# Kernel tuning notes

Hardware: AMD Instinct MI355X
Metric: run time of the kernel (lower is better)

Reference implementation:

```python
import jax, jax.numpy as jnp
import numpy as np

NS, NM, NR, H = 5000, 100000, 2000, 128
E_SM, E_RM, E_SIM, L = 2_000_000, 1_000_000, 2_000_000, 500_000
NUM_LAYERS = 4  # flattened: layer-0 sage convs 0..3, layer-1 sage convs 0..3 -> stacked [2,4,...]


def _seg_sum(x, idx, n):
    return jax.ops.segment_sum(x, idx, num_segments=n)


def sage_conv(x_src, x_dst, Wl, bl, Wr, src, dst, n_dst):
    # PyG SAGEConv: mean-aggregate neighbor features, lin_l (with bias), + lin_r(root, no bias)
    agg = _seg_sum(x_src[src], dst, n_dst)                      # [n_dst, H]
    cnt = _seg_sum(jnp.ones_like(src, dtype=x_src.dtype), dst, n_dst)
    mean = agg / jnp.maximum(cnt, 1.0)[:, None]
    return mean @ Wl + bl + x_dst @ Wr


def gcn_conv(x, W, b, src, dst, n):
    # PyG GCNConv: add self loops, symmetric normalization deg^-1/2 (deg over dst incl. self loops)
    loop = jnp.arange(n, dtype=src.dtype)
    src2 = jnp.concatenate([src, loop])
    dst2 = jnp.concatenate([dst, loop])
    deg = _seg_sum(jnp.ones_like(dst2, dtype=x.dtype), dst2, n)
    dinv = jnp.where(deg > 0, jax.lax.rsqrt(deg), 0.0)
    norm = dinv[src2] * dinv[dst2]                               # [E+n]
    xw = x @ W                                                   # [n, H]
    out = _seg_sum(xw[src2] * norm[:, None], dst2, n)
    return out + b


def setup_inputs() -> dict:
    key = jax.random.key(0)
    ks = jax.random.split(key, 20)
    s = 0.05
    inp = {
        "emb_srna": jax.random.normal(ks[0], (NS, H), jnp.float32) * s,
        "emb_mrna": jax.random.normal(ks[1], (NM, H), jnp.float32) * s,
        "emb_rbp": jax.random.normal(ks[2], (NR, H), jnp.float32) * s,
        # stacked SAGE params: [layer=2, rel=4, ...]; rel order:
        # 0: srna->mrna, 1: mrna->srna (rev), 2: rbp->mrna, 3: mrna->rbp (rev)
        "sage_Wl": jax.random.normal(ks[3], (2, 4, H, H), jnp.float32) * s,
        "sage_bl": jnp.zeros((2, 4, H), jnp.float32),
        "sage_Wr": jax.random.normal(ks[4], (2, 4, H, H), jnp.float32) * s,
        # stacked GCN params: [layer=2, rel=2 (sim, rev_sim), ...]
        "gcn_W": jax.random.normal(ks[5], (2, 2, H, H), jnp.float32) * s,
        "gcn_b": jnp.zeros((2, 2, H), jnp.float32),
        "src_sm": jax.random.randint(ks[6], (E_SM,), 0, NS),
        "dst_sm": jax.random.randint(ks[7], (E_SM,), 0, NM),
        "src_rm": jax.random.randint(ks[8], (E_RM,), 0, NR),
        "dst_rm": jax.random.randint(ks[9], (E_RM,), 0, NM),
        "src_sim": jax.random.randint(ks[10], (E_SIM,), 0, NM),
        "dst_sim": jax.random.randint(ks[11], (E_SIM,), 0, NM),
        "lbl_srna": jax.random.randint(ks[12], (L,), 0, NS),
        "lbl_mrna": jax.random.randint(ks[13], (L,), 0, NM),
        "lbl_rbp": jax.random.randint(ks[14], (L,), 0, NR),
    }
    return inp


def reference(emb_srna, emb_mrna, emb_rbp, sage_Wl, sage_bl, sage_Wr, gcn_W, gcn_b,
              src_sm, dst_sm, src_rm, dst_rm, src_sim, dst_sim,
              lbl_srna, lbl_mrna, lbl_rbp):
    x_s, x_m, x_r = emb_srna, emb_mrna, emb_rbp
    for l in range(2):
        m_new = (
            sage_conv(x_s, x_m, sage_Wl[l, 0], sage_bl[l, 0], sage_Wr[l, 0], src_sm, dst_sm, NM)
            + sage_conv(x_r, x_m, sage_Wl[l, 2], sage_bl[l, 2], sage_Wr[l, 2], src_rm, dst_rm, NM)
            + gcn_conv(x_m, gcn_W[l, 0], gcn_b[l, 0], src_sim, dst_sim, NM)
            + gcn_conv(x_m, gcn_W[l, 1], gcn_b[l, 1], dst_sim, src_sim, NM)
        )
        s_new = sage_conv(x_m, x_s, sage_Wl[l, 1], sage_bl[l, 1], sage_Wr[l, 1], dst_sm, src_sm, NS)
        r_new = sage_conv(x_m, x_r, sage_Wl[l, 3], sage_bl[l, 3], sage_Wr[l, 3], dst_rm, src_rm, NR)
        x_s, x_m, x_r = jax.nn.relu(s_new), jax.nn.relu(m_new), jax.nn.relu(r_new)
    feat_m = x_m[lbl_mrna]
    pred_srna_mrna = jnp.sum(x_s[lbl_srna] * feat_m, axis=-1)
    pred_rbp_mrna = jnp.sum(x_r[lbl_rbp] * feat_m, axis=-1)
    return (pred_srna_mrna, pred_rbp_mrna)
```

## Files before the change

### kernel.cpp

```cpp
#include <hip/hip_runtime.h>
#include <hip/hip_bf16.h>

#define NSN 5000
#define NMN 100000
#define NRN 2000
#define HDIM 128
#define ESM 2000000
#define ERM 1000000
#define ESIM 2000000
#define LBL 500000

#define CNT_TOTAL (4 * NMN + NSN + NRN)
#define POOL_TOTAL (2 * ESM + 2 * ERM + 2 * ESIM)
#define NBTOT 1222
#define WCAP 14336
#define MAXNODES 512
#define MBLK 25000
#define SR_TOTAL (NSN + NRN)

#define CAP0 12288
#define CAP1 8192
#define CAP2 7168
#define CAP3 9216
#define CAP4 12288
#define CAP5 12288
#define PB0 0
#define PB1 (PB0 + 196 * CAP0)
#define PB2 (PB1 + 313 * CAP1)
#define PB3 (PB2 + 196 * CAP2)
#define PB4 (PB3 + 125 * CAP3)
#define PB5 (PB4 + 196 * CAP4)

typedef short bf16x8 __attribute__((ext_vector_type(8)));
typedef float f32x4 __attribute__((ext_vector_type(4)));
typedef float f32x2 __attribute__((ext_vector_type(2)));

__device__ __forceinline__ unsigned short f2bf(float f) {
  unsigned u = __float_as_uint(f);
  unsigned r = (u + 0x7fffu + ((u >> 16) & 1u)) >> 16;
  return (unsigned short)r;
}
__device__ __forceinline__ float bf_lo(unsigned v) { return __uint_as_float(v << 16); }
__device__ __forceinline__ float bf_hi(unsigned v) { return __uint_as_float(v & 0xffff0000u); }
__device__ __forceinline__ unsigned pack2(float x, float y) {
  return (unsigned)f2bf(x) | ((unsigned)f2bf(y) << 16);
}
__device__ __forceinline__ f32x2 up2(unsigned v) {
  f32x2 r;
  r.x = bf_lo(v);
  r.y = bf_hi(v);
  return r;
}
__device__ __forceinline__ void unpack8(uint4 v, float* f) {
  f[0] = bf_lo(v.x); f[1] = bf_hi(v.x);
  f[2] = bf_lo(v.y); f[3] = bf_hi(v.y);
  f[4] = bf_lo(v.z); f[5] = bf_hi(v.z);
  f[6] = bf_lo(v.w); f[7] = bf_hi(v.w);
}


__global__ void zero_int(int* __restrict__ p, int n) {
  int i = blockIdx.x * blockDim.x + threadIdx.x;
  if (i < n) p[i] = 0;
}

struct BInfo { int g; int ns; int ne; };
__device__ __forceinline__ BInfo binfo(int id) {
  BInfo bi;
  if (id < 196)       { int k = id;        bi.g = 0;                   bi.ns = k << 9; bi.ne = min(bi.ns + 512, NMN); }
  else if (id < 509)  { int k = id - 196;  bi.g = NMN;                 bi.ns = k << 4; bi.ne = min(bi.ns + 16,  NSN); }
  else if (id < 705)  { int k = id - 509;  bi.g = NMN + NSN;           bi.ns = k << 9; bi.ne = min(bi.ns + 512, NMN); }
  else if (id < 830)  { int k = id - 705;  bi.g = 2 * NMN + NSN;       bi.ns = k << 4; bi.ne = min(bi.ns + 16,  NRN); }
  else if (id < 1026) { int k = id - 830;  bi.g = 2 * NMN + NSN + NRN; bi.ns = k << 9; bi.ne = min(bi.ns + 512, NMN); }
  else                { int k = id - 1026; bi.g = 3 * NMN + NSN + NRN; bi.ns = k << 9; bi.ne = min(bi.ns + 512, NMN); }
  return bi;
}

__device__ __forceinline__ int pstart(int id) {
  if (id < 196)       return PB0 + id * CAP0;
  else if (id < 509)  return PB1 + (id - 196) * CAP1;
  else if (id < 705)  return PB2 + (id - 509) * CAP2;
  else if (id < 830)  return PB3 + (id - 705) * CAP3;
  else if (id < 1026) return PB4 + (id - 830) * CAP4;
  else                return PB5 + (id - 1026) * CAP5;
}

__global__ void init_pcur(int* __restrict__ bcur) {
  int id = blockIdx.x * blockDim.x + threadIdx.x;
  if (id < NBTOT) bcur[id] = pstart(id);
}

template <int SHF, int NBF, int SHR, int NBR>
__global__ __launch_bounds__(256) void multisplit(
    const int* __restrict__ a, const int* __restrict__ b, int n,
    int* __restrict__ bcur, int bb, int2* __restrict__ stage) {
  __shared__ int hist[NBF + NBR];
  __shared__ int gpos[NBF + NBR];
  int tid = threadIdx.x;
  int base = blockIdx.x * 4096;
  for (int k = tid; k < NBF + NBR; k += 256) hist[k] = 0;
  __syncthreads();
  int dv[16], sv[16];
#pragma unroll
  for (int j = 0; j < 16; j++) {
    int idx = base + j * 256 + tid;
    if (idx < n) {
      sv[j] = a[idx]; dv[j] = b[idx];
      atomicAdd(&hist[dv[j] >> SHF], 1);
      atomicAdd(&hist[NBF + (sv[j] >> SHR)], 1);
    } else {
      dv[j] = -1;
    }
  }
  __syncthreads();
  for (int k = tid; k < NBF + NBR; k += 256) {
    int c = hist[k];
    gpos[k] = c ? atomicAdd(&bcur[bb + k], c) : 0;
  }
  __syncthreads();
#pragma unroll
  for (int j = 0; j < 16; j++) {
    if (dv[j] >= 0) {
      int s1 = atomicAdd(&gpos[dv[j] >> SHF], 1);
      stage[s1] = make_int2(dv[j], sv[j]);
      int s2 = atomicAdd(&gpos[NBF + (sv[j] >> SHR)], 1);
      stage[s2] = make_int2(sv[j], dv[j]);
    }
  }
}

__global__ void scan_counts(const int* __restrict__ bcur, int* __restrict__ bstart,
                            int* __restrict__ off_sentinel) {
  __shared__ int buf[256];
  int t = threadIdx.x;
  int base = 0;
  for (int c0 = 0; c0 < NBTOT; c0 += 256) {
    int id = c0 + t;
    int v = (id < NBTOT) ? (bcur[id] - pstart(id)) : 0;
    buf[t] = v; __syncthreads();
    for (int o = 1; o < 256; o <<= 1) {
      int a = (t >= o) ? buf[t - o] : 0;
      __syncthreads();
      buf[t] += a;
      __syncthreads();
    }
    if (id < NBTOT) bstart[id] = buf[t] - v + base;
    base += buf[255];
    __syncthreads();
  }
  if (t == 0) { bstart[NBTOT] = base; *off_sentinel = base; }
}

__global__ __launch_bounds__(256) void scatter_bucket(
    const int2* __restrict__ stage, const int* __restrict__ bstart,
    int* __restrict__ cur, int* __restrict__ off, int* __restrict__ pool) {
  __shared__ int win[WCAP];
  __shared__ int hist[MAXNODES];
  __shared__ int part[256];
  int b = blockIdx.x;
  BInfo bi = binfo(b);
  int p0 = pstart(b);
  int d0 = bstart[b];
  int sz = bstart[b + 1] - d0;
  int nn = bi.ne - bi.ns;
  int t = threadIdx.x;
  for (int k = t; k < nn; k += 256) hist[k] = 0;
  __syncthreads();
  for (int k = t; k < sz; k += 256)
    atomicAdd(&hist[stage[p0 + k].x - bi.ns], 1);
  __syncthreads();
  int a0 = (2 * t < nn) ? hist[2 * t] : 0;
  int a1 = (2 * t + 1 < nn) ? hist[2 * t + 1] : 0;
  part[t] = a0 + a1;
  __syncthreads();
  for (int o = 1; o < 256; o <<= 1) {
    int a = (t >= o) ? part[t - o] : 0;
    __syncthreads();
    part[t] += a;
    __syncthreads();
  }
  int e0 = part[t] - a0 - a1;
  int e1 = e0 + a0;
  if (2 * t < nn)     { off[bi.g + bi.ns + 2 * t] = d0 + e0; hist[2 * t] = e0; }
  if (2 * t + 1 < nn) { off[bi.g + bi.ns + 2 * t + 1] = d0 + e1; hist[2 * t + 1] = e1; }
  __syncthreads();
  if (sz <= WCAP) {
    for (int k = t; k < sz; k += 256) {
      int2 pr = stage[p0 + k];
      int slot = atomicAdd(&hist[pr.x - bi.ns], 1);
      win[slot] = pr.y;
    }
    __syncthreads();
    for (int k = t; k < sz; k += 256) pool[d0 + k] = win[k];
  } else {
    for (int k = t; k < sz; k += 256) {
      int2 pr = stage[p0 + k];
      int slot = atomicAdd(&cur[bi.g + pr.x], 1);
      pool[d0 + hist[pr.x - bi.ns] + slot] = pr.y;
    }
  }
}

__global__ void compute_dinv(const int* __restrict__ off1, const int* __restrict__ off2,
                             float* __restrict__ dinv1, float* __restrict__ dinv2, int n) {
  int v = blockIdx.x * blockDim.x + threadIdx.x;
  if (v < n) {
    dinv1[v] = rsqrtf((float)(off1[v + 1] - off1[v] + 1));
    dinv2[v] = rsqrtf((float)(off2[v + 1] - off2[v] + 1));
  }
}

__global__ void trans_weights(const float* __restrict__ sWl, const float* __restrict__ sWr,
                              const float* __restrict__ gW, unsigned short* __restrict__ wt) {
  int i = blockIdx.x * blockDim.x + threadIdx.x;
  if (i >= 18 * 16384) return;
  int mat = i >> 14, l = mat / 9, slot = mat % 9;
  int idx = i & 16383, nn = idx >> 7, kk = idx & 127;
  int s_ = kk * 128 + nn;
  float v;
  if (slot < 4)      v = sWl[((l * 4 + slot) << 14) + s_];
  else if (slot < 6) v = gW[((l * 2 + (slot - 4)) << 14) + s_];
  else if (slot == 6) v = sWr[((l * 4 + 0) << 14) + s_] + sWr[((l * 4 + 2) << 14) + s_];
  else if (slot == 7) v = sWr[((l * 4 + 1) << 14) + s_];
  else                v = sWr[((l * 4 + 3) << 14) + s_];
  wt[i] = f2bf(v);
}

__global__ void prep_bias(const float* __restrict__ sbl, const float* __restrict__ gb,
                          float* __restrict__ biasM) {
  int i = threadIdx.x;
  int l = i >> 7, j = i & 127;
  biasM[i] = sbl[(l * 4 + 0) * 128 + j] + sbl[(l * 4 + 2) * 128 + j] +
             gb[(l * 2 + 0) * 128 + j] + gb[(l * 2 + 1) * 128 + j];
}

__global__ void cast_all(const float2* __restrict__ es, const float2* __restrict__ em,
                         const float2* __restrict__ er, unsigned* __restrict__ os,
                         unsigned* __restrict__ om, unsigned* __restrict__ orr) {
  int i = blockIdx.x * blockDim.x + threadIdx.x;
  if (i < NSN * 64) { float2 v = es[i]; os[i] = pack2(v.x, v.y); }
  if (i < NMN * 64) { float2 v = em[i]; om[i] = pack2(v.x, v.y); }
  if (i < NRN * 64) { float2 v = er[i]; orr[i] = pack2(v.x, v.y); }
}


__device__ __forceinline__ void body_plain16(const unsigned* __restrict__ xh,
                                             const int* __restrict__ pool,
                                             int i0, int q, f32x2* acc) {
  int u1 = pool[i0 + q], u2 = pool[i0 + 4 + q];
  int u3 = pool[i0 + 8 + q], u4 = pool[i0 + 12 + q];
  uint4 a = *(const uint4*)(xh + (size_t)u1 * 64);
  uint4 b = *(const uint4*)(xh + (size_t)u2 * 64);
  uint4 c = *(const uint4*)(xh + (size_t)u3 * 64);
  uint4 d = *(const uint4*)(xh + (size_t)u4 * 64);
  acc[0] += up2(a.x) * 1.f + up2(b.x) * 1.f + up2(c.x) * 1.f + up2(d.x) * 1.f;
  acc[1] += up2(a.y) * 1.f + up2(b.y) * 1.f + up2(c.y) * 1.f + up2(d.y) * 1.f;
  acc[2] += up2(a.z) * 1.f + up2(b.z) * 1.f + up2(c.z) * 1.f + up2(d.z) * 1.f;
  acc[3] += up2(a.w) * 1.f + up2(b.w) * 1.f + up2(c.w) * 1.f + up2(d.w) * 1.f;
}

__device__ __forceinline__ void body_gcn16(const unsigned* __restrict__ xh,
                                           const int* __restrict__ pool,
                                           const float* __restrict__ dinv,
                                           int i0, int q, f32x2* acc) {
  int u1 = pool[i0 + q], u2 = pool[i0 + 4 + q];
  int u3 = pool[i0 + 8 + q], u4 = pool[i0 + 12 + q];
  uint4 a = *(const uint4*)(xh + (size_t)u1 * 64);
  uint4 b = *(const uint4*)(xh + (size_t)u2 * 64);
  uint4 c = *(const uint4*)(xh + (size_t)u3 * 64);
  uint4 d = *(const uint4*)(xh + (size_t)u4 * 64);
  float s1 = dinv[u1], s2 = dinv[u2], s3 = dinv[u3], s4 = dinv[u4];
  acc[0] += up2(a.x) * s1 + up2(b.x) * s2 + up2(c.x) * s3 + up2(d.x) * s4;
  acc[1] += up2(a.y) * s1 + up2(b.y) * s2 + up2(c.y) * s3 + up2(d.y) * s4;
  acc[2] += up2(a.z) * s1 + up2(b.z) * s2 + up2(c.z) * s3 + up2(d.z) * s4;
  acc[3] += up2(a.w) * s1 + up2(b.w) * s2 + up2(c.w) * s3 + up2(d.w) * s4;
}

__device__ __forceinline__ void tail_plain16(const unsigned* __restrict__ xh,
                                             const int* __restrict__ pool,
                                             int i0, int e, int q, f32x2* acc) {
  int i1 = i0 + q, i2 = i0 + 4 + q, i3 = i0 + 8 + q, i4 = i0 + 12 + q;
  int u1 = pool[min(i1, e - 1)], u2 = pool[min(i2, e - 1)];
  int u3 = pool[min(i3, e - 1)], u4 = pool[min(i4, e - 1)];
  uint4 a = *(const uint4*)(xh + (size_t)u1 * 64);
  uint4 b = *(const uint4*)(xh + (size_t)u2 * 64);
  uint4 c = *(const uint4*)(xh + (size_t)u3 * 64);
  uint4 d = *(const uint4*)(xh + (size_t)u4 * 64);
  float s1 = (i1 < e) ? 1.f : 0.f, s2 = (i2 < e) ? 1.f : 0.f;
  float s3 = (i3 < e) ? 1.f : 0.f, s4 = (i4 < e) ? 1.f : 0.f;
  acc[0] += up2(a.x) * s1 + up2(b.x) * s2 + up2(c.x) * s3 + up2(d.x) * s4;
  acc[1] += up2(a.y) * s1 + up2(b.y) * s2 + up2(c.y) * s3 + up2(d.y) * s4;
  acc[2] += up2(a.z) * s1 + up2(b.z) * s2 + up2(c.z) * s3 + up2(d.z) * s4;
  acc[3] += up2(a.w) * s1 + up2(b.w) * s2 + up2(c.w) * s3 + up2(d.w) * s4;
}

__device__ __forceinline__ void tail_gcn16(const unsigned* __restrict__ xh,
                                           const int* __restrict__ pool,
                                           const float* __restrict__ dinv,
                                           int i0, int e, int q, f32x2* acc) {
  int i1 = i0 + q, i2 = i0 + 4 + q, i3 = i0 + 8 + q, i4 = i0 + 12 + q;
  int u1 = pool[min(i1, e - 1)], u2 = pool[min(i2, e - 1)];
  int u3 = pool[min(i3, e - 1)], u4 = pool[min(i4, e - 1)];
  uint4 a = *(const uint4*)(xh + (size_t)u1 * 64);
  uint4 b = *(const uint4*)(xh + (size_t)u2 * 64);
  uint4 c = *(const uint4*)(xh + (size_t)u3 * 64);
  uint4 d = *(const uint4*)(xh + (size_t)u4 * 64);
  float s1 = (i1 < e) ? dinv[u1] : 0.f, s2 = (i2 < e) ? dinv[u2] : 0.f;
  float s3 = (i3 < e) ? dinv[u3] : 0.f, s4 = (i4 < e) ? dinv[u4] : 0.f;
  acc[0] += up2(a.x) * s1 + up2(b.x) * s2 + up2(c.x) * s3 + up2(d.x) * s4;
  acc[1] += up2(a.y) * s1 + up2(b.y) * s2 + up2(c.y) * s3 + up2(d.y) * s4;
  acc[2] += up2(a.z) * s1 + up2(b.z) * s2 + up2(c.z) * s3 + up2(d.z) * s4;
  acc[3] += up2(a.w) * s1 + up2(b.w) * s2 + up2(c.w) * s3 + up2(d.w) * s4;
}

__device__ __forceinline__ void wave_reduce2(f32x2* acc) {
#pragma unroll
  for (int j = 0; j < 4; j++) {
    acc[j].x += __shfl_xor(acc[j].x, 16, 64);
    acc[j].y += __shfl_xor(acc[j].y, 16, 64);
    acc[j].x += __shfl_xor(acc[j].x, 32, 64);
    acc[j].y += __shfl_xor(acc[j].y, 32, 64);
  }
}

__device__ __forceinline__ uint4 pack_scaled(const f32x2* acc, float sc) {
  uint4 o;
  o.x = pack2(acc[0].x * sc, acc[0].y * sc);
  o.y = pack2(acc[1].x * sc, acc[1].y * sc);
  o.z = pack2(acc[2].x * sc, acc[2].y * sc);
  o.w = pack2(acc[3].x * sc, acc[3].y * sc);
  return o;
}

__global__ __launch_bounds__(256) void agg_all(
    const unsigned* __restrict__ xs, const unsigned* __restrict__ xm,
    const unsigned* __restrict__ xr, const int* __restrict__ pool,
    const int* __restrict__ off_sm, const int* __restrict__ off_rm,
    const int* __restrict__ off_si, const int* __restrict__ off_si2,
    const int* __restrict__ off_ms, const int* __restrict__ off_mr,
    const float* __restrict__ dinv1, const float* __restrict__ dinv2,
    unsigned* __restrict__ aggA, unsigned* __restrict__ aggB,
    unsigned* __restrict__ aggC, unsigned* __restrict__ aggD,
    unsigned* __restrict__ aggS, unsigned* __restrict__ aggR) {
  __shared__ float psum[3][128];
  int b = blockIdx.x;
  int lane = threadIdx.x & 63;
  int q = lane >> 4, h = lane & 15;

  int k4 = b >> 2, r4 = b & 3;
  bool is_sr = (r4 == 3) && (k4 < SR_TOTAL);

  if (!is_sr) {
    int mb = b - min(k4 + ((r4 == 3) ? 1 : 0), SR_TOTAL);
    int w = mb * 4 + (threadIdx.x >> 6);
    if (w >= NMN) return;
    const unsigned* xsh = xs + h * 4;
    const unsigned* xmh = xm + h * 4;
    const unsigned* xrh = xr + h * 4;
    f32x2 acc[4];
    {
      int s = off_sm[w], e = off_sm[w + 1];
      int nb = (e - s) & ~15;
#pragma unroll
      for (int j = 0; j < 4; j++) acc[j] = (f32x2)(0.f);
      int i0 = s;
      for (; i0 < s + nb; i0 += 16) body_plain16(xsh, pool, i0, q, acc);
      if (i0 < e) tail_plain16(xsh, pool, i0, e, q, acc);
      wave_reduce2(acc);
      if (q == 0) {
        float inv = (e > s) ? 1.0f / (float)(e - s) : 0.0f;
        *(uint4*)(aggA + (size_t)w * 64 + h * 4) = pack_scaled(acc, inv);
      }
    }
    {
      int s = off_rm[w], e = off_rm[w + 1];
      int nb = (e - s) & ~15;
#pragma unroll
      for (int j = 0; j < 4; j++) acc[j] = (f32x2)(0.f);
      int i0 = s;
      for (; i0 < s + nb; i0 += 16) body_plain16(xrh, pool, i0, q, acc);
      if (i0 < e) tail_plain16(xrh, pool, i0, e, q, acc);
      wave_reduce2(acc);
      if (q == 0) {
        float inv = (e > s) ? 1.0f / (float)(e - s) : 0.0f;
        *(uint4*)(aggB + (size_t)w * 64 + h * 4) = pack_scaled(acc, inv);
      }
    }
    {
      int s = off_si[w], e = off_si[w + 1];
      int nb = (e - s) & ~15;
#pragma unroll
      for (int j = 0; j < 4; j++) acc[j] = (f32x2)(0.f);
      int i0 = s;
      for (; i0 < s + nb; i0 += 16) body_gcn16(xmh, pool, dinv1, i0, q, acc);
      if (i0 < e) tail_gcn16(xmh, pool, dinv1, i0, e, q, acc);
      wave_reduce2(acc);
      if (q == 0) {
        float dw = dinv1[w];
        uint4 xv = *(const uint4*)(xmh + (size_t)w * 64);
        f32x2 fx[4] = {up2(xv.x), up2(xv.y), up2(xv.z), up2(xv.w)};
        float dw2 = dw * dw;
        uint4 o;
        f32x2 r0 = acc[0] * dw + fx[0] * dw2, r1 = acc[1] * dw + fx[1] * dw2;
        f32x2 r2 = acc[2] * dw + fx[2] * dw2, r3 = acc[3] * dw + fx[3] * dw2;
        o.x = pack2(r0.x, r0.y); o.y = pack2(r1.x, r1.y);
        o.z = pack2(r2.x, r2.y); o.w = pack2(r3.x, r3.y);
        *(uint4*)(aggC + (size_t)w * 64 + h * 4) = o;
      }
    }
    {
      int s = off_si2[w], e = off_si2[w + 1];
      int nb = (e - s) & ~15;
#pragma unroll
      for (int j = 0; j < 4; j++) acc[j] = (f32x2)(0.f);
      int i0 = s;
      for (; i0 < s + nb; i0 += 16) body_gcn16(xmh, pool, dinv2, i0, q, acc);
      if (i0 < e) tail_gcn16(xmh, pool, dinv2, i0, e, q, acc);
      wave_reduce2(acc);
      if (q == 0) {
        float dw = dinv2[w];
        uint4 xv = *(const uint4*)(xmh + (size_t)w * 64);
        f32x2 fx[4] = {up2(xv.x), up2(xv.y), up2(xv.z), up2(xv.w)};
        float dw2 = dw * dw;
        uint4 o;
        f32x2 r0 = acc[0] * dw + fx[0] * dw2, r1 = acc[1] * dw + fx[1] * dw2;
        f32x2 r2 = acc[2] * dw + fx[2] * dw2, r3 = acc[3] * dw + fx[3] * dw2;
        o.x = pack2(r0.x, r0.y); o.y = pack2(r1.x, r1.y);
        o.z = pack2(r2.x, r2.y); o.w = pack2(r3.x, r3.y);
        *(uint4*)(aggD + (size_t)w * 64 + h * 4) = o;
      }
    }
  } else {
    int sr = k4;
    int node;
    const int* offp;
    unsigned* outb;
    if (sr < NSN) { node = sr; offp = off_ms; outb = aggS; }
    else          { node = sr - NSN; offp = off_mr; outb = aggR; }
    const unsigned* xmh = xm + h * 4;
    int sub = threadIdx.x >> 6;
    int s = offp[node], e = offp[node + 1];
    f32x2 acc[4];
#pragma unroll
    for (int j = 0; j < 4; j++) acc[j] = (f32x2)(0.f);
    int i0 = s + sub * 16;
    for (; i0 + 16 <= e; i0 += 64) body_plain16(xmh, pool, i0, q, acc);
    if (i0 < e) tail_plain16(xmh, pool, i0, e, q, acc);
    wave_reduce2(acc);
    if (sub && q == 0) {
#pragma unroll
      for (int j = 0; j < 4; j++) {
        psum[sub - 1][h * 8 + 2 * j] = acc[j].x;
        psum[sub - 1][h * 8 + 2 * j + 1] = acc[j].y;
      }
    }
    __syncthreads();
    if (sub == 0 && q == 0) {
#pragma unroll
      for (int j = 0; j < 4; j++) {
        acc[j].x += psum[0][h * 8 + 2 * j] + psum[1][h * 8 + 2 * j] + psum[2][h * 8 + 2 * j];
        acc[j].y += psum[0][h * 8 + 2 * j + 1] + psum[1][h * 8 + 2 * j + 1] + psum[2][h * 8 + 2 * j + 1];
      }
      float inv = (e > s) ? 1.0f / (float)(e - s) : 0.0f;
      *(uint4*)(outb + (size_t)node * 64 + h * 4) = pack_scaled(acc, inv);
    }
  }
}


#define LDA 136

__global__ __launch_bounds__(256) void gemm_mfma(
    const unsigned short* __restrict__ a0, const unsigned short* __restrict__ w0,
    const unsigned short* __restrict__ a1, const unsigned short* __restrict__ w1,
    const unsigned short* __restrict__ a2, const unsigned short* __restrict__ w2,
    const unsigned short* __restrict__ a3, const unsigned short* __restrict__ w3,
    const unsigned short* __restrict__ a4, const unsigned short* __restrict__ w4,
    const float* __restrict__ bias, unsigned short* __restrict__ out, int n) {
  __shared__ __align__(16) unsigned short As[64 * LDA];
  __shared__ __align__(16) unsigned short Ws[128 * LDA];

  int tid = threadIdx.x;
  int w = tid >> 6, lane = tid & 63;
  int q = lane >> 4, c = lane & 15;
  int r0 = blockIdx.x * 64;

  const unsigned short* Ap[5] = {a0, a1, a2, a3, a4};
  const unsigned short* Wp[5] = {w0, w1, w2, w3, w4};

  float bias_v[8];
#pragma unroll
  for (int n0 = 0; n0 < 8; n0++) bias_v[n0] = bias[n0 * 16 + c];

  f32x4 acc[8];
#pragma unroll
  for (int n0 = 0; n0 < 8; n0++) acc[n0] = (f32x4){0.f, 0.f, 0.f, 0.f};

  for (int p = 0; p < 5; p++) {
    if (!Ap[p]) continue;
    __syncthreads();
    for (int j = tid; j < 2048; j += 256) {
      int row = j >> 4, colc = (j & 15) * 8;
      *(uint4*)&Ws[row * LDA + colc] = *(const uint4*)(Wp[p] + row * 128 + colc);
    }
    for (int j = tid; j < 1024; j += 256) {
      int row = j >> 4, colc = (j & 15) * 8;
      uint4 v = make_uint4(0u, 0u, 0u, 0u);
      if (r0 + row < n) v = *(const uint4*)(Ap[p] + (size_t)(r0 + row) * 128 + colc);
      *(uint4*)&As[row * LDA + colc] = v;
    }
    __syncthreads();

    int arow = (w * 16 + c) * LDA;
#pragma unroll
    for (int k0 = 0; k0 < 128; k0 += 32) {
      bf16x8 af = *(const bf16x8*)&As[arow + k0 + q * 8];
#pragma unroll
      for (int n0 = 0; n0 < 8; n0++) {
        bf16x8 bfv = *(const bf16x8*)&Ws[(n0 * 16 + c) * LDA + k0 + q * 8];
        acc[n0] = __builtin_amdgcn_mfma_f32_16x16x32_bf16(af, bfv, acc[n0], 0, 0, 0);
      }
    }
  }

  __syncthreads();
#pragma unroll
  for (int n0 = 0; n0 < 8; n0++) {
#pragma unroll
    for (int reg = 0; reg < 4; reg++) {
      float v = acc[n0][reg] + bias_v[n0];
      v = fmaxf(v, 0.f);
      As[(w * 16 + q * 4 + reg) * LDA + n0 * 16 + c] = f2bf(v);
    }
  }
  __syncthreads();
  for (int j = tid; j < 1024; j += 256) {
    int row = j >> 4, colc = (j & 15) * 8;
    if (r0 + row < n)
      *(uint4*)(out + (size_t)(r0 + row) * 128 + colc) = *(const uint4*)&As[row * LDA + colc];
  }
}


__global__ void dots_kernel(const unsigned* __restrict__ xs, const unsigned* __restrict__ xm,
                            const unsigned* __restrict__ xr, const int* __restrict__ ls,
                            const int* __restrict__ lm, const int* __restrict__ lr,
                            float* __restrict__ out) {
  int wv = (blockIdx.x * blockDim.x + threadIdx.x) >> 6;
  int lane = threadIdx.x & 63;
  int q = lane >> 4, h = lane & 15;
  int i = wv * 4 + q;
  if (i >= LBL) return;
  int im = lm[i], is = ls[i], ir = lr[i];
  uint4 mv = *(const uint4*)(xm + (size_t)im * 64 + h * 4);
  uint4 sv = *(const uint4*)(xs + (size_t)is * 64 + h * 4);
  uint4 rv = *(const uint4*)(xr + (size_t)ir * 64 + h * 4);
  float fm[8], fs[8], fr[8];
  unpack8(mv, fm); unpack8(sv, fs); unpack8(rv, fr);
  float p1 = 0.f, p2 = 0.f;
#pragma unroll
  for (int j = 0; j < 8; j++) { p1 = fmaf(fs[j], fm[j], p1); p2 = fmaf(fr[j], fm[j], p2); }
#pragma unroll
  for (int m = 1; m < 16; m <<= 1) {
    p1 += __shfl_xor(p1, m, 64);
    p2 += __shfl_xor(p2, m, 64);
  }
  if (h == 0) { out[i] = p1; out[LBL + i] = p2; }
}


extern "C" void kernel_launch(void* const* d_in, const int* in_sizes, int n_in,
                              void* d_out, int out_size, void* d_ws, size_t ws_size,
                              hipStream_t stream) {
  const float* emb_s = (const float*)d_in[0];
  const float* emb_m = (const float*)d_in[1];
  const float* emb_r = (const float*)d_in[2];
  const float* sWl = (const float*)d_in[3];
  const float* sbl = (const float*)d_in[4];
  const float* sWr = (const float*)d_in[5];
  const float* gW  = (const float*)d_in[6];
  const float* gb  = (const float*)d_in[7];
  const int* src_sm  = (const int*)d_in[8];
  const int* dst_sm  = (const int*)d_in[9];
  const int* src_rm  = (const int*)d_in[10];
  const int* dst_rm  = (const int*)d_in[11];
  const int* src_sim = (const int*)d_in[12];
  const int* dst_sim = (const int*)d_in[13];
  const int* lbl_s = (const int*)d_in[14];
  const int* lbl_m = (const int*)d_in[15];
  const int* lbl_r = (const int*)d_in[16];
  float* out = (float*)d_out;

  char* p = (char*)d_ws;
  auto alloc = [&](size_t bytes) -> char* {
    char* r = p;
    p += (bytes + 255) & ~(size_t)255;
    return r;
  };

  int* cnt_base = (int*)alloc(sizeof(int) * CNT_TOTAL);

  int* off_base = (int*)alloc(sizeof(int) * (CNT_TOTAL + 1));
  int* off_sm  = off_base;
  int* off_ms  = off_sm + NMN;
  int* off_rm  = off_ms + NSN;
  int* off_mr  = off_rm + NMN;
  int* off_si  = off_mr + NRN;
  int* off_si2 = off_si + NMN;

  int* bstart = (int*)alloc(sizeof(int) * 1280);
  int* bcur   = (int*)alloc(sizeof(int) * 1280);
  int* pool = (int*)alloc(sizeof(int) * POOL_TOTAL);

  float* dinv1 = (float*)alloc(sizeof(float) * NMN);
  float* dinv2 = (float*)alloc(sizeof(float) * NMN);

  unsigned* xsb = (unsigned*)alloc(sizeof(unsigned) * (size_t)NSN * 64);
  unsigned* xmb = (unsigned*)alloc(sizeof(unsigned) * (size_t)NMN * 64);
  unsigned* xrb = (unsigned*)alloc(sizeof(unsigned) * (size_t)NRN * 64);
  unsigned* xs0 = (unsigned*)alloc(sizeof(unsigned) * (size_t)NSN * 64);
  unsigned* xs1 = (unsigned*)alloc(sizeof(unsigned) * (size_t)NSN * 64);
  unsigned* xm0 = (unsigned*)alloc(sizeof(unsigned) * (size_t)NMN * 64);
  unsigned* xm1 = (unsigned*)alloc(sizeof(unsigned) * (size_t)NMN * 64);
  unsigned* xr0 = (unsigned*)alloc(sizeof(unsigned) * (size_t)NRN * 64);
  unsigned* xr1 = (unsigned*)alloc(sizeof(unsigned) * (size_t)NRN * 64);
  unsigned* aggA = (unsigned*)alloc(sizeof(unsigned) * (size_t)NMN * 64);
  unsigned* aggB = (unsigned*)alloc(sizeof(unsigned) * (size_t)NMN * 64);
  unsigned* aggC = (unsigned*)alloc(sizeof(unsigned) * (size_t)NMN * 64);
  unsigned* aggD = (unsigned*)alloc(sizeof(unsigned) * (size_t)NMN * 64);
  unsigned* aggS = (unsigned*)alloc(sizeof(unsigned) * (size_t)NSN * 64);
  unsigned* aggR = (unsigned*)alloc(sizeof(unsigned) * (size_t)NRN * 64);

  unsigned short* wt = (unsigned short*)alloc(sizeof(unsigned short) * 18 * 16384);
  float* biasM = (float*)alloc(sizeof(float) * 2 * 128);

  int2* stage = (int2*)aggA;

  auto WT = [&](int l, int slot) -> const unsigned short* {
    return wt + (((size_t)l * 9 + slot) << 14);
  };

  init_pcur<<<(NBTOT + 255) / 256, 256, 0, stream>>>(bcur);
  multisplit<9, 196, 4, 313><<<(ESM + 4095) / 4096, 256, 0, stream>>>(
      src_sm, dst_sm, ESM, bcur, 0, stage);
  multisplit<9, 196, 4, 125><<<(ERM + 4095) / 4096, 256, 0, stream>>>(
      src_rm, dst_rm, ERM, bcur, 509, stage);
  multisplit<9, 196, 9, 196><<<(ESIM + 4095) / 4096, 256, 0, stream>>>(
      src_sim, dst_sim, ESIM, bcur, 830, stage);
  scan_counts<<<1, 256, 0, stream>>>(bcur, bstart, off_base + CNT_TOTAL);
  zero_int<<<(CNT_TOTAL + 255) / 256, 256, 0, stream>>>(cnt_base, CNT_TOTAL);
  scatter_bucket<<<NBTOT, 256, 0, stream>>>(stage, bstart, cnt_base, off_base, pool);

  compute_dinv<<<(NMN + 255) / 256, 256, 0, stream>>>(off_si, off_si2, dinv1, dinv2, NMN);
  trans_weights<<<(18 * 16384 + 255) / 256, 256, 0, stream>>>(sWl, sWr, gW, wt);
  prep_bias<<<1, 256, 0, stream>>>(sbl, gb, biasM);
  cast_all<<<(NMN * 64 + 255) / 256, 256, 0, stream>>>((const float2*)emb_s, (const float2*)emb_m,
                                                       (const float2*)emb_r, xsb, xmb, xrb);

  const int AGG_GRID = MBLK + SR_TOTAL;
  for (int l = 0; l < 2; ++l) {
    const unsigned* xs_c = l ? xs0 : xsb;
    const unsigned* xm_c = l ? xm0 : xmb;
    const unsigned* xr_c = l ? xr0 : xrb;
    unsigned* xs_n = l ? xs1 : xs0;
    unsigned* xm_n = l ? xm1 : xm0;
    unsigned* xr_n = l ? xr1 : xr0;

    agg_all<<<AGG_GRID, 256, 0, stream>>>(
        xs_c, xm_c, xr_c, pool, off_sm, off_rm, off_si, off_si2, off_ms, off_mr,
        dinv1, dinv2, aggA, aggB, aggC, aggD, aggS, aggR);

    gemm_mfma<<<(NMN + 63) / 64, 256, 0, stream>>>(
        (const unsigned short*)aggA, WT(l, 0), (const unsigned short*)aggB, WT(l, 2),
        (const unsigned short*)aggC, WT(l, 4), (const unsigned short*)aggD, WT(l, 5),
        (const unsigned short*)xm_c, WT(l, 6), biasM + l * 128,
        (unsigned short*)xm_n, NMN);
    gemm_mfma<<<(NSN + 63) / 64, 256, 0, stream>>>(
        (const unsigned short*)aggS, WT(l, 1), (const unsigned short*)xs_c, WT(l, 7),
        nullptr, nullptr, nullptr, nullptr, nullptr, nullptr,
        sbl + (l * 4 + 1) * 128, (unsigned short*)xs_n, NSN);
    gemm_mfma<<<(NRN + 63) / 64, 256, 0, stream>>>(
        (const unsigned short*)aggR, WT(l, 3), (const unsigned short*)xr_c, WT(l, 8),
        nullptr, nullptr, nullptr, nullptr, nullptr, nullptr,
        sbl + (l * 4 + 3) * 128, (unsigned short*)xr_n, NRN);
  }

  dots_kernel<<<(LBL * 16 + 255) / 256, 256, 0, stream>>>(xs1, xm1, xr1, lbl_s, lbl_m, lbl_r, out);
}
```

Baseline: 1.092 ms.

## Restructure aggregation to one wave per node with readlane-broadcast neighbor indices

The aggregation kernel is rewritten so that each wave handles one destination node, and each lane owns 2 of the 128 features. The wave loads up to 64 neighbor indices (and GCN scales) cooperatively, then broadcasts them with readlane and gathers 4-byte slices per lane. This replaces the old scheme, where quarter-waves read 16-byte chunks and were combined with a cross-lane shuffle reduction, and sRNA/RBP nodes used block-level shared-memory reductions. The aim is to drop the reduction and shuffle overhead and give uniform per-node work. The cost is narrower 4-byte gathers per lane and serialized readlane loops, and high-degree sRNA/RBP nodes now run on a single wave instead of four.

```diff
diff --git a/kernel.cpp b/kernel.cpp
--- a/kernel.cpp
+++ b/kernel.cpp
@@ -15,7 +15,6 @@
 #define NBTOT 1222
 #define WCAP 14336
 #define MAXNODES 512
-#define MBLK 25000
 #define SR_TOTAL (NSN + NRN)
 
 #define CAP0 12288
@@ -44,12 +43,6 @@
 __device__ __forceinline__ float bf_hi(unsigned v) { return __uint_as_float(v & 0xffff0000u); }
 __device__ __forceinline__ unsigned pack2(float x, float y) {
   return (unsigned)f2bf(x) | ((unsigned)f2bf(y) << 16);
-}
-__device__ __forceinline__ f32x2 up2(unsigned v) {
-  f32x2 r;
-  r.x = bf_lo(v);
-  r.y = bf_hi(v);
-  return r;
 }
 __device__ __forceinline__ void unpack8(uint4 v, float* f) {
   f[0] = bf_lo(v.x); f[1] = bf_hi(v.x);
@@ -244,92 +237,73 @@
 }
 
 
-__device__ __forceinline__ void body_plain16(const unsigned* __restrict__ xh,
-                                             const int* __restrict__ pool,
-                                             int i0, int q, f32x2* acc) {
-  int u1 = pool[i0 + q], u2 = pool[i0 + 4 + q];
-  int u3 = pool[i0 + 8 + q], u4 = pool[i0 + 12 + q];
-  uint4 a = *(const uint4*)(xh + (size_t)u1 * 64);
-  uint4 b = *(const uint4*)(xh + (size_t)u2 * 64);
-  uint4 c = *(const uint4*)(xh + (size_t)u3 * 64);
-  uint4 d = *(const uint4*)(xh + (size_t)u4 * 64);
-  acc[0] += up2(a.x) * 1.f + up2(b.x) * 1.f + up2(c.x) * 1.f + up2(d.x) * 1.f;
-  acc[1] += up2(a.y) * 1.f + up2(b.y) * 1.f + up2(c.y) * 1.f + up2(d.y) * 1.f;
-  acc[2] += up2(a.z) * 1.f + up2(b.z) * 1.f + up2(c.z) * 1.f + up2(d.z) * 1.f;
-  acc[3] += up2(a.w) * 1.f + up2(b.w) * 1.f + up2(c.w) * 1.f + up2(d.w) * 1.f;
-}
-
-__device__ __forceinline__ void body_gcn16(const unsigned* __restrict__ xh,
-                                           const int* __restrict__ pool,
-                                           const float* __restrict__ dinv,
-                                           int i0, int q, f32x2* acc) {
-  int u1 = pool[i0 + q], u2 = pool[i0 + 4 + q];
-  int u3 = pool[i0 + 8 + q], u4 = pool[i0 + 12 + q];
-  uint4 a = *(const uint4*)(xh + (size_t)u1 * 64);
-  uint4 b = *(const uint4*)(xh + (size_t)u2 * 64);
-  uint4 c = *(const uint4*)(xh + (size_t)u3 * 64);
-  uint4 d = *(const uint4*)(xh + (size_t)u4 * 64);
-  float s1 = dinv[u1], s2 = dinv[u2], s3 = dinv[u3], s4 = dinv[u4];
-  acc[0] += up2(a.x) * s1 + up2(b.x) * s2 + up2(c.x) * s3 + up2(d.x) * s4;
-  acc[1] += up2(a.y) * s1 + up2(b.y) * s2 + up2(c.y) * s3 + up2(d.y) * s4;
-  acc[2] += up2(a.z) * s1 + up2(b.z) * s2 + up2(c.z) * s3 + up2(d.z) * s4;
-  acc[3] += up2(a.w) * s1 + up2(b.w) * s2 + up2(c.w) * s3 + up2(d.w) * s4;
-}
-
-__device__ __forceinline__ void tail_plain16(const unsigned* __restrict__ xh,
-                                             const int* __restrict__ pool,
-                                             int i0, int e, int q, f32x2* acc) {
-  int i1 = i0 + q, i2 = i0 + 4 + q, i3 = i0 + 8 + q, i4 = i0 + 12 + q;
-  int u1 = pool[min(i1, e - 1)], u2 = pool[min(i2, e - 1)];
-  int u3 = pool[min(i3, e - 1)], u4 = pool[min(i4, e - 1)];
-  uint4 a = *(const uint4*)(xh + (size_t)u1 * 64);
-  uint4 b = *(const uint4*)(xh + (size_t)u2 * 64);
-  uint4 c = *(const uint4*)(xh + (size_t)u3 * 64);
-  uint4 d = *(const uint4*)(xh + (size_t)u4 * 64);
-  float s1 = (i1 < e) ? 1.f : 0.f, s2 = (i2 < e) ? 1.f : 0.f;
-  float s3 = (i3 < e) ? 1.f : 0.f, s4 = (i4 < e) ? 1.f : 0.f;
-  acc[0] += up2(a.x) * s1 + up2(b.x) * s2 + up2(c.x) * s3 + up2(d.x) * s4;
-  acc[1] += up2(a.y) * s1 + up2(b.y) * s2 + up2(c.y) * s3 + up2(d.y) * s4;
-  acc[2] += up2(a.z) * s1 + up2(b.z) * s2 + up2(c.z) * s3 + up2(d.z) * s4;
-  acc[3] += up2(a.w) * s1 + up2(b.w) * s2 + up2(c.w) * s3 + up2(d.w) * s4;
-}
-
-__device__ __forceinline__ void tail_gcn16(const unsigned* __restrict__ xh,
-                                           const int* __restrict__ pool,
-                                           const float* __restrict__ dinv,
-                                           int i0, int e, int q, f32x2* acc) {
-  int i1 = i0 + q, i2 = i0 + 4 + q, i3 = i0 + 8 + q, i4 = i0 + 12 + q;
-  int u1 = pool[min(i1, e - 1)], u2 = pool[min(i2, e - 1)];
-  int u3 = pool[min(i3, e - 1)], u4 = pool[min(i4, e - 1)];
-  uint4 a = *(const uint4*)(xh + (size_t)u1 * 64);
-  uint4 b = *(const uint4*)(xh + (size_t)u2 * 64);
-  uint4 c = *(const uint4*)(xh + (size_t)u3 * 64);
-  uint4 d = *(const uint4*)(xh + (size_t)u4 * 64);
-  float s1 = (i1 < e) ? dinv[u1] : 0.f, s2 = (i2 < e) ? dinv[u2] : 0.f;
-  float s3 = (i3 < e) ? dinv[u3] : 0.f, s4 = (i4 < e) ? dinv[u4] : 0.f;
-  acc[0] += up2(a.x) * s1 + up2(b.x) * s2 + up2(c.x) * s3 + up2(d.x) * s4;
-  acc[1] += up2(a.y) * s1 + up2(b.y) * s2 + up2(c.y) * s3 + up2(d.y) * s4;
-  acc[2] += up2(a.z) * s1 + up2(b.z) * s2 + up2(c.z) * s3 + up2(d.z) * s4;
-  acc[3] += up2(a.w) * s1 + up2(b.w) * s2 + up2(c.w) * s3 + up2(d.w) * s4;
-}
-
-__device__ __forceinline__ void wave_reduce2(f32x2* acc) {
-#pragma unroll
-  for (int j = 0; j < 4; j++) {
-    acc[j].x += __shfl_xor(acc[j].x, 16, 64);
-    acc[j].y += __shfl_xor(acc[j].y, 16, 64);
-    acc[j].x += __shfl_xor(acc[j].x, 32, 64);
-    acc[j].y += __shfl_xor(acc[j].y, 32, 64);
-  }
-}
-
-__device__ __forceinline__ uint4 pack_scaled(const f32x2* acc, float sc) {
-  uint4 o;
-  o.x = pack2(acc[0].x * sc, acc[0].y * sc);
-  o.y = pack2(acc[1].x * sc, acc[1].y * sc);
-  o.z = pack2(acc[2].x * sc, acc[2].y * sc);
-  o.w = pack2(acc[3].x * sc, acc[3].y * sc);
-  return o;
+template <bool GCN>
+__device__ __forceinline__ f32x2 agg_list(const char* __restrict__ xb,
+                                          const int* __restrict__ pool,
+                                          const float* __restrict__ dinv,
+                                          int s, int e, int l4) {
+  f32x2 a0 = (f32x2)(0.f), a1 = (f32x2)(0.f);
+  if (e <= s) return a0;
+  for (int i0 = s; i0 < e; i0 += 64) {
+    int cnt = min(64, e - i0);
+    int pidx = min(i0 + (l4 >> 2), e - 1);
+    int pv = pool[pidx];
+    float dvv = 0.f;
+    if (GCN) dvv = dinv[pv];
+    int k = 0;
+    for (; k + 16 <= cnt; k += 16) {
+      unsigned vv[16];
+      float sc[16];
+#pragma unroll
+      for (int j = 0; j < 16; j++) {
+        int u = __builtin_amdgcn_readlane(pv, k + j);
+        if (GCN)
+          sc[j] = __uint_as_float(
+              (unsigned)__builtin_amdgcn_readlane((int)__float_as_uint(dvv), k + j));
+        vv[j] = *(const unsigned*)(xb + (((unsigned)u << 8) + (unsigned)l4));
+      }
+#pragma unroll
+      for (int j = 0; j < 16; j++) {
+        float m = GCN ? sc[j] : 1.0f;
+        if (j & 1) {
+          a1.x = fmaf(bf_lo(vv[j]), m, a1.x);
+          a1.y = fmaf(bf_hi(vv[j]), m, a1.y);
+        } else {
+          a0.x = fmaf(bf_lo(vv[j]), m, a0.x);
+          a0.y = fmaf(bf_hi(vv[j]), m, a0.y);
+        }
+      }
+    }
+    if (k < cnt) {
+      unsigned vv[16];
+      float sc[16];
+#pragma unroll
+      for (int j = 0; j < 16; j++) {
+        int kk = min(k + j, cnt - 1);
+        int u = __builtin_amdgcn_readlane(pv, kk);
+        float m;
+        if (k + j < cnt)
+          m = GCN ? __uint_as_float(
+                        (unsigned)__builtin_amdgcn_readlane((int)__float_as_uint(dvv), kk))
+                  : 1.0f;
+        else
+          m = 0.0f;
+        sc[j] = m;
+        vv[j] = *(const unsigned*)(xb + (((unsigned)u << 8) + (unsigned)l4));
+      }
+#pragma unroll
+      for (int j = 0; j < 16; j++) {
+        if (j & 1) {
+          a1.x = fmaf(bf_lo(vv[j]), sc[j], a1.x);
+          a1.y = fmaf(bf_hi(vv[j]), sc[j], a1.y);
+        } else {
+          a0.x = fmaf(bf_lo(vv[j]), sc[j], a0.x);
+          a0.y = fmaf(bf_hi(vv[j]), sc[j], a0.y);
+        }
+      }
+    }
+  }
+  return a0 + a1;
 }
 
 __global__ __launch_bounds__(256) void agg_all(
@@ -342,127 +316,53 @@
     unsigned* __restrict__ aggA, unsigned* __restrict__ aggB,
     unsigned* __restrict__ aggC, unsigned* __restrict__ aggD,
     unsigned* __restrict__ aggS, unsigned* __restrict__ aggR) {
-  __shared__ float psum[3][128];
-  int b = blockIdx.x;
-  int lane = threadIdx.x & 63;
-  int q = lane >> 4, h = lane & 15;
-
-  int k4 = b >> 2, r4 = b & 3;
-  bool is_sr = (r4 == 3) && (k4 < SR_TOTAL);
-
-  if (!is_sr) {
-    int mb = b - min(k4 + ((r4 == 3) ? 1 : 0), SR_TOTAL);
-    int w = mb * 4 + (threadIdx.x >> 6);
-    if (w >= NMN) return;
-    const unsigned* xsh = xs + h * 4;
-    const unsigned* xmh = xm + h * 4;
-    const unsigned* xrh = xr + h * 4;
-    f32x2 acc[4];
-    {
-      int s = off_sm[w], e = off_sm[w + 1];
-      int nb = (e - s) & ~15;
-#pragma unroll
-      for (int j = 0; j < 4; j++) acc[j] = (f32x2)(0.f);
-      int i0 = s;
-      for (; i0 < s + nb; i0 += 16) body_plain16(xsh, pool, i0, q, acc);
-      if (i0 < e) tail_plain16(xsh, pool, i0, e, q, acc);
-      wave_reduce2(acc);
-      if (q == 0) {
-        float inv = (e > s) ? 1.0f / (float)(e - s) : 0.0f;
-        *(uint4*)(aggA + (size_t)w * 64 + h * 4) = pack_scaled(acc, inv);
-      }
-    }
-    {
-      int s = off_rm[w], e = off_rm[w + 1];
-      int nb = (e - s) & ~15;
-#pragma unroll
-      for (int j = 0; j < 4; j++) acc[j] = (f32x2)(0.f);
-      int i0 = s;
-      for (; i0 < s + nb; i0 += 16) body_plain16(xrh, pool, i0, q, acc);
-      if (i0 < e) tail_plain16(xrh, pool, i0, e, q, acc);
-      wave_reduce2(acc);
-      if (q == 0) {
-        float inv = (e > s) ? 1.0f / (float)(e - s) : 0.0f;
-        *(uint4*)(aggB + (size_t)w * 64 + h * 4) = pack_scaled(acc, inv);
-      }
-    }
-    {
-      int s = off_si[w], e = off_si[w + 1];
-      int nb = (e - s) & ~15;
-#pragma unroll
-      for (int j = 0; j < 4; j++) acc[j] = (f32x2)(0.f);
-      int i0 = s;
-      for (; i0 < s + nb; i0 += 16) body_gcn16(xmh, pool, dinv1, i0, q, acc);
-      if (i0 < e) tail_gcn16(xmh, pool, dinv1, i0, e, q, acc);
-      wave_reduce2(acc);
-      if (q == 0) {
-        float dw = dinv1[w];
-        uint4 xv = *(const uint4*)(xmh + (size_t)w * 64);
-        f32x2 fx[4] = {up2(xv.x), up2(xv.y), up2(xv.z), up2(xv.w)};
-        float dw2 = dw * dw;
-        uint4 o;
-        f32x2 r0 = acc[0] * dw + fx[0] * dw2, r1 = acc[1] * dw + fx[1] * dw2;
-        f32x2 r2 = acc[2] * dw + fx[2] * dw2, r3 = acc[3] * dw + fx[3] * dw2;
-        o.x = pack2(r0.x, r0.y); o.y = pack2(r1.x, r1.y);
-        o.z = pack2(r2.x, r2.y); o.w = pack2(r3.x, r3.y);
-        *(uint4*)(aggC + (size_t)w * 64 + h * 4) = o;
-      }
-    }
-    {
-      int s = off_si2[w], e = off_si2[w + 1];
-      int nb = (e - s) & ~15;
-#pragma unroll
-      for (int j = 0; j < 4; j++) acc[j] = (f32x2)(0.f);
-      int i0 = s;
-      for (; i0 < s + nb; i0 += 16) body_gcn16(xmh, pool, dinv2, i0, q, acc);
-      if (i0 < e) tail_gcn16(xmh, pool, dinv2, i0, e, q, acc);
-      wave_reduce2(acc);
-      if (q == 0) {
-        float dw = dinv2[w];
-        uint4 xv = *(const uint4*)(xmh + (size_t)w * 64);
-        f32x2 fx[4] = {up2(xv.x), up2(xv.y), up2(xv.z), up2(xv.w)};
-        float dw2 = dw * dw;
-        uint4 o;
-        f32x2 r0 = acc[0] * dw + fx[0] * dw2, r1 = acc[1] * dw + fx[1] * dw2;
-        f32x2 r2 = acc[2] * dw + fx[2] * dw2, r3 = acc[3] * dw + fx[3] * dw2;
-        o.x = pack2(r0.x, r0.y); o.y = pack2(r1.x, r1.y);
-        o.z = pack2(r2.x, r2.y); o.w = pack2(r3.x, r3.y);
-        *(uint4*)(aggD + (size_t)w * 64 + h * 4) = o;
-      }
-    }
-  } else {
-    int sr = k4;
+  int wv = blockIdx.x * 4 + (threadIdx.x >> 6);
+  wv = __builtin_amdgcn_readfirstlane(wv);
+  int l = threadIdx.x & 63;
+  int l4 = l << 2;
+
+  if (wv < SR_TOTAL) {
     int node;
     const int* offp;
     unsigned* outb;
-    if (sr < NSN) { node = sr; offp = off_ms; outb = aggS; }
-    else          { node = sr - NSN; offp = off_mr; outb = aggR; }
-    const unsigned* xmh = xm + h * 4;
-    int sub = threadIdx.x >> 6;
+    if (wv < NSN) { node = wv; offp = off_ms; outb = aggS; }
+    else          { node = wv - NSN; offp = off_mr; outb = aggR; }
     int s = offp[node], e = offp[node + 1];
-    f32x2 acc[4];
-#pragma unroll
-    for (int j = 0; j < 4; j++) acc[j] = (f32x2)(0.f);
-    int i0 = s + sub * 16;
-    for (; i0 + 16 <= e; i0 += 64) body_plain16(xmh, pool, i0, q, acc);
-    if (i0 < e) tail_plain16(xmh, pool, i0, e, q, acc);
-    wave_reduce2(acc);
-    if (sub && q == 0) {
-#pragma unroll
-      for (int j = 0; j < 4; j++) {
-        psum[sub - 1][h * 8 + 2 * j] = acc[j].x;
-        psum[sub - 1][h * 8 + 2 * j + 1] = acc[j].y;
-      }
-    }
-    __syncthreads();
-    if (sub == 0 && q == 0) {
-#pragma unroll
-      for (int j = 0; j < 4; j++) {
-        acc[j].x += psum[0][h * 8 + 2 * j] + psum[1][h * 8 + 2 * j] + psum[2][h * 8 + 2 * j];
-        acc[j].y += psum[0][h * 8 + 2 * j + 1] + psum[1][h * 8 + 2 * j + 1] + psum[2][h * 8 + 2 * j + 1];
-      }
-      float inv = (e > s) ? 1.0f / (float)(e - s) : 0.0f;
-      *(uint4*)(outb + (size_t)node * 64 + h * 4) = pack_scaled(acc, inv);
+    f32x2 a = agg_list<false>((const char*)xm, pool, nullptr, s, e, l4);
+    float inv = (e > s) ? 1.0f / (float)(e - s) : 0.0f;
+    outb[(size_t)node * 64 + l] = pack2(a.x * inv, a.y * inv);
+  } else {
+    int w = wv - SR_TOTAL;
+    int sA = off_sm[w],  eA = off_sm[w + 1];
+    int sB = off_rm[w],  eB = off_rm[w + 1];
+    int sC = off_si[w],  eC = off_si[w + 1];
+    int sD = off_si2[w], eD = off_si2[w + 1];
+    unsigned xv = xm[(size_t)w * 64 + l];
+    float dw1 = dinv1[w], dw2_ = dinv2[w];
+
+    {
+      f32x2 a = agg_list<false>((const char*)xs, pool, nullptr, sA, eA, l4);
+      float inv = (eA > sA) ? 1.0f / (float)(eA - sA) : 0.0f;
+      aggA[(size_t)w * 64 + l] = pack2(a.x * inv, a.y * inv);
+    }
+    {
+      f32x2 a = agg_list<false>((const char*)xr, pool, nullptr, sB, eB, l4);
+      float inv = (eB > sB) ? 1.0f / (float)(eB - sB) : 0.0f;
+      aggB[(size_t)w * 64 + l] = pack2(a.x * inv, a.y * inv);
+    }
+    {
+      f32x2 a = agg_list<true>((const char*)xm, pool, dinv1, sC, eC, l4);
+      float dsq = dw1 * dw1;
+      float rx = a.x * dw1 + bf_lo(xv) * dsq;
+      float ry = a.y * dw1 + bf_hi(xv) * dsq;
+      aggC[(size_t)w * 64 + l] = pack2(rx, ry);
+    }
+    {
+      f32x2 a = agg_list<true>((const char*)xm, pool, dinv2, sD, eD, l4);
+      float dsq = dw2_ * dw2_;
+      float rx = a.x * dw2_ + bf_lo(xv) * dsq;
+      float ry = a.y * dw2_ + bf_hi(xv) * dsq;
+      aggD[(size_t)w * 64 + l] = pack2(rx, ry);
     }
   }
 }
@@ -657,7 +557,7 @@
   cast_all<<<(NMN * 64 + 255) / 256, 256, 0, stream>>>((const float2*)emb_s, (const float2*)emb_m,
                                                        (const float2*)emb_r, xsb, xmb, xrb);
 
-  const int AGG_GRID = MBLK + SR_TOTAL;
+  const int AGG_GRID = (SR_TOTAL + NMN) / 4;
   for (int l = 0; l < 2; ++l) {
     const unsigned* xs_c = l ? xs0 : xsb;
     const unsigned* xm_c = l ? xm0 : xmb;
```

Result: no change. 1.091 ms (-0.2%).
